# Performance work log

Hardware: AMD Instinct MI355X
Metric: run time of the kernel (lower is better)

## Reference

```python
import jax, jax.numpy as jnp
import numpy as np

K_SIZE = 5  # local window size (odd, SAME padding, stride 1)


def _local_attn(x_main, x_ref, W_main, W_ref, k_size=K_SIZE):
    # 1x1 convs == per-pixel channel matmuls
    cm = jnp.einsum('bhwc,cd->bhwd', x_main, W_main)  # query  [B,H,W,C']
    cr = jnp.einsum('bhwc,cd->bhwd', x_ref, W_ref)    # keys   [B,H,W,C']
    pad = (k_size - 1) // 2
    B, H, W, C = cr.shape
    crp = jnp.pad(cr, ((0, 0), (pad, pad), (pad, pad), (0, 0)))
    # score for each of the k*k offsets: dot(query, shifted key) per pixel.
    # Avoids materializing the [B,H,W,k*k,C] patch tensor.
    scores = [
        jnp.einsum('bhwc,bhwc->bhw', cm, crp[:, i:i + H, j:j + W, :])
        for i in range(k_size) for j in range(k_size)
    ]
    # the layer concatenates the query itself as the last "key" (self score)
    scores.append(jnp.einsum('bhwc,bhwc->bhw', cm, cm))
    attn = jnp.stack(scores, axis=-1)  # [B,H,W,k*k+1]
    return jax.nn.softmax(attn, axis=-1)


def setup_inputs() -> dict:
    key = jax.random.key(0)
    k1, k2, k3, k4 = jax.random.split(key, 4)
    B, H, W, C = 4, 128, 128, 64
    Ci = 64  # intermediate_dim
    return {
        'x_main': jax.random.normal(k1, (B, H, W, C), jnp.float32),
        'x_ref': jax.random.normal(k2, (B, H, W, C), jnp.float32),
        'W_main': jax.random.normal(k3, (C, Ci), jnp.float32) * (2.0 / C) ** 0.5,
        'W_ref': jax.random.normal(k4, (C, Ci), jnp.float32) * (2.0 / C) ** 0.5,
    }


def reference(x_main, x_ref, W_main, W_ref):
    return _local_attn(x_main, x_ref, W_main, W_ref)
```

## Files before the change

kernel.cpp:

```cpp
#include <hip/hip_runtime.h>
#include <math.h>

#define HDIM 128
#define WDIM 128
#define CDIM 64
#define BDIM 4

#define TILE_W 16
#define TILE_H 8
#define HALO_W 20
#define HALO_H 12
#define NHALO (HALO_W * HALO_H)
#define PSTRIDE 68

typedef short bf16x8 __attribute__((ext_vector_type(8)));
typedef float f32x4  __attribute__((ext_vector_type(4)));

__device__ __forceinline__ void split_bf16(float f, short& hi, short& lo) {
    unsigned u = __float_as_uint(f);
    hi = (short)(u >> 16);
    float hf = __uint_as_float(u & 0xffff0000u);
    float l  = f - hf;
    lo = (short)(__float_as_uint(l) >> 16);
}

__device__ __forceinline__ void build_A(const float4 p0, const float4 p1,
                                        const float4 p2, const float4 p3,
                                        bf16x8 Ahi[2], bf16x8 Alo[2]) {
    float fv[16] = {p0.x,p0.y,p0.z,p0.w, p1.x,p1.y,p1.z,p1.w,
                    p2.x,p2.y,p2.z,p2.w, p3.x,p3.y,p3.z,p3.w};
    #pragma unroll
    for (int ks = 0; ks < 2; ++ks)
        #pragma unroll
        for (int j = 0; j < 8; ++j) {
            short hi, lo; split_bf16(fv[8 * ks + j], hi, lo);
            Ahi[ks][j] = hi; Alo[ks][j] = lo;
        }
}

__global__ __launch_bounds__(256, 2)
void fused_mfma_local_attn(const float* __restrict__ xm,
                           const float* __restrict__ xr,
                           const float* __restrict__ Wm,
                           const float* __restrict__ Wr,
                           float* __restrict__ out) {
    __shared__ float lds[16320];
    float* cms = lds;
    float* crs = lds;

    const int t    = threadIdx.x;
    const int lane = t & 63;
    const int wv   = t >> 6;
    const int m    = lane & 15;
    const int quad = lane >> 4;
    const int tx0  = blockIdx.x * TILE_W;
    const int ty0  = blockIdx.y * TILE_H;
    const int b    = blockIdx.z;

    float4 am[2][4];
    #pragma unroll
    for (int s = 0; s < 2; ++s) {
        const int tile = 2 * wv + s;
        const float* ap = xm + (((size_t)b * HDIM + ty0 + tile) * WDIM
                                + tx0 + m) * CDIM + quad * 8;
        am[s][0] = *(const float4*)(ap);
        am[s][1] = *(const float4*)(ap + 4);
        am[s][2] = *(const float4*)(ap + 32);
        am[s][3] = *(const float4*)(ap + 36);
    }

    float4 ar[2][4];
    #pragma unroll
    for (int s = 0; s < 2; ++s) {
        const int tj = wv + 4 * s;
        const int hp = tj * 16 + m;
        const int hy = hp / HALO_W;
        const int hx = hp - hy * HALO_W;
        const int gy = ty0 + hy - 2, gx = tx0 + hx - 2;
        float4 z = make_float4(0.f, 0.f, 0.f, 0.f);
        ar[s][0] = z; ar[s][1] = z; ar[s][2] = z; ar[s][3] = z;
        if (gy >= 0 && gy < HDIM && gx >= 0 && gx < WDIM) {
            const float* ap = xr + (((size_t)b * HDIM + gy) * WDIM + gx) * CDIM
                              + quad * 8;
            ar[s][0] = *(const float4*)(ap);
            ar[s][1] = *(const float4*)(ap + 4);
            ar[s][2] = *(const float4*)(ap + 32);
            ar[s][3] = *(const float4*)(ap + 36);
        }
    }

    bf16x8 Bhi[2][4], Blo[2][4];
    #pragma unroll
    for (int ks = 0; ks < 2; ++ks)
        #pragma unroll
        for (int nt = 0; nt < 4; ++nt)
            #pragma unroll
            for (int j = 0; j < 8; ++j) {
                float f = Wm[(ks * 32 + quad * 8 + j) * CDIM + nt * 16 + m];
                short hi, lo; split_bf16(f, hi, lo);
                Bhi[ks][nt][j] = hi; Blo[ks][nt][j] = lo;
            }

    #pragma unroll
    for (int s = 0; s < 2; ++s) {
        const int tile = 2 * wv + s;
        bf16x8 Ahi[2], Alo[2];
        build_A(am[s][0], am[s][1], am[s][2], am[s][3], Ahi, Alo);
        f32x4 acc[4];
        #pragma unroll
        for (int nt = 0; nt < 4; ++nt)
            { acc[nt][0]=0.f; acc[nt][1]=0.f; acc[nt][2]=0.f; acc[nt][3]=0.f; }
        #pragma unroll
        for (int ks = 0; ks < 2; ++ks)
            #pragma unroll
            for (int nt = 0; nt < 4; ++nt) {
                acc[nt] = __builtin_amdgcn_mfma_f32_16x16x32_bf16(Ahi[ks], Bhi[ks][nt], acc[nt], 0,0,0);
                acc[nt] = __builtin_amdgcn_mfma_f32_16x16x32_bf16(Ahi[ks], Blo[ks][nt], acc[nt], 0,0,0);
                acc[nt] = __builtin_amdgcn_mfma_f32_16x16x32_bf16(Alo[ks], Bhi[ks][nt], acc[nt], 0,0,0);
            }
        #pragma unroll
        for (int nt = 0; nt < 4; ++nt)
            #pragma unroll
            for (int r = 0; r < 4; ++r)
                cms[(tile * 16 + quad * 4 + r) * PSTRIDE + nt * 16 + m] = acc[nt][r];
    }

    const int pl = t >> 1;
    const int cg = t & 1;
    float4 qv[8];
    #pragma unroll
    for (int mq = 0; mq < 8; ++mq)
        qv[mq] = *(const float4*)&cms[pl * PSTRIDE + cg * 32 + 4 * mq];

    float4 ar2[2][4];
    #pragma unroll
    for (int s = 0; s < 2; ++s) {
        const int tj = wv + 4 * (s + 2);
        float4 z = make_float4(0.f, 0.f, 0.f, 0.f);
        ar2[s][0] = z; ar2[s][1] = z; ar2[s][2] = z; ar2[s][3] = z;
        if (tj < 15) {
            const int hp = tj * 16 + m;
            const int hy = hp / HALO_W;
            const int hx = hp - hy * HALO_W;
            const int gy = ty0 + hy - 2, gx = tx0 + hx - 2;
            if (gy >= 0 && gy < HDIM && gx >= 0 && gx < WDIM) {
                const float* ap = xr + (((size_t)b * HDIM + gy) * WDIM + gx) * CDIM
                                  + quad * 8;
                ar2[s][0] = *(const float4*)(ap);
                ar2[s][1] = *(const float4*)(ap + 4);
                ar2[s][2] = *(const float4*)(ap + 32);
                ar2[s][3] = *(const float4*)(ap + 36);
            }
        }
    }

    #pragma unroll
    for (int ks = 0; ks < 2; ++ks)
        #pragma unroll
        for (int nt = 0; nt < 4; ++nt)
            #pragma unroll
            for (int j = 0; j < 8; ++j) {
                float f = Wr[(ks * 32 + quad * 8 + j) * CDIM + nt * 16 + m];
                short hi, lo; split_bf16(f, hi, lo);
                Bhi[ks][nt][j] = hi; Blo[ks][nt][j] = lo;
            }

    __syncthreads();

    #pragma unroll
    for (int s = 0; s < 4; ++s) {
        const int tj = wv + 4 * s;
        if (tj < 15) {
            const float4* pa = (s < 2) ? ar[s] : ar2[s - 2];
            bf16x8 Ahi[2], Alo[2];
            build_A(pa[0], pa[1], pa[2], pa[3], Ahi, Alo);
            f32x4 acc[4];
            #pragma unroll
            for (int nt = 0; nt < 4; ++nt)
                { acc[nt][0]=0.f; acc[nt][1]=0.f; acc[nt][2]=0.f; acc[nt][3]=0.f; }
            #pragma unroll
            for (int ks = 0; ks < 2; ++ks)
                #pragma unroll
                for (int nt = 0; nt < 4; ++nt) {
                    acc[nt] = __builtin_amdgcn_mfma_f32_16x16x32_bf16(Ahi[ks], Bhi[ks][nt], acc[nt], 0,0,0);
                    acc[nt] = __builtin_amdgcn_mfma_f32_16x16x32_bf16(Ahi[ks], Blo[ks][nt], acc[nt], 0,0,0);
                    acc[nt] = __builtin_amdgcn_mfma_f32_16x16x32_bf16(Alo[ks], Bhi[ks][nt], acc[nt], 0,0,0);
                }
            #pragma unroll
            for (int nt = 0; nt < 4; ++nt)
                #pragma unroll
                for (int r = 0; r < 4; ++r)
                    crs[(tj * 16 + quad * 4 + r) * PSTRIDE + nt * 16 + m] = acc[nt][r];
        }
    }
    __syncthreads();

    const int lx = pl & (TILE_W - 1);
    const int ly = pl >> 4;
    const size_t gpx = ((size_t)b * HDIM + ty0 + ly) * WDIM + tx0 + lx;

    float s[26];
    #pragma unroll
    for (int k = 0; k < 25; ++k) {
        const int i = k / 5, j = k % 5;
        const int p = (ly + i) * HALO_W + (lx + j);
        const float4* kp = (const float4*)&crs[p * PSTRIDE + cg * 32];
        float acc = 0.f;
        #pragma unroll
        for (int mq = 0; mq < 8; ++mq) {
            float4 v = kp[mq];
            acc = fmaf(qv[mq].x, v.x, acc);
            acc = fmaf(qv[mq].y, v.y, acc);
            acc = fmaf(qv[mq].z, v.z, acc);
            acc = fmaf(qv[mq].w, v.w, acc);
        }
        s[k] = acc;
    }
    {
        float acc = 0.f;
        #pragma unroll
        for (int mq = 0; mq < 8; ++mq) {
            float4 v = qv[mq];
            acc = fmaf(v.x, v.x, acc);
            acc = fmaf(v.y, v.y, acc);
            acc = fmaf(v.z, v.z, acc);
            acc = fmaf(v.w, v.w, acc);
        }
        s[25] = acc;
    }

    #pragma unroll
    for (int k = 0; k < 26; ++k) s[k] += __shfl_xor(s[k], 1);

    float mx = s[0];
    #pragma unroll
    for (int k = 1; k < 26; ++k) mx = fmaxf(mx, s[k]);
    float sum = 0.f;
    #pragma unroll
    for (int k = 0; k < 26; ++k) { s[k] = __expf(s[k] - mx); sum += s[k]; }
    const float inv = 1.f / sum;

    float* op = &out[gpx * 26 + cg * 13];
    if (cg == 0) {
        #pragma unroll
        for (int k = 0; k < 13; ++k) op[k] = s[k] * inv;
    } else {
        #pragma unroll
        for (int k = 0; k < 13; ++k) op[k] = s[13 + k] * inv;
    }
}

extern "C" void kernel_launch(void* const* d_in, const int* in_sizes, int n_in,
                              void* d_out, int out_size, void* d_ws, size_t ws_size,
                              hipStream_t stream) {
    const float* xm = (const float*)d_in[0];
    const float* xr = (const float*)d_in[1];
    const float* Wm = (const float*)d_in[2];
    const float* Wr = (const float*)d_in[3];
    float* outp = (float*)d_out;

    dim3 g(WDIM / TILE_W, HDIM / TILE_H, BDIM);
    fused_mfma_local_attn<<<g, 256, 0, stream>>>(xm, xr, Wm, Wr, outp);
}
```

Measured before the change: 91.75 us.

## Halve tile height and split channel dot products across four lanes per pixel

The output tile height drops from 8 to 4 rows, so the halo shrinks to 20x8 and the grid has twice as many blocks. Each pixel's 64-channel dot products are now split over four lanes of 16 channels instead of two of 32, reduced with an extra xor shuffle, and each lane writes a quarter of the outputs. Launch bounds ask for 3 blocks per CU. This cuts per-thread register use and LDS size to raise occupancy, at the cost of more redundant halo projection work per output (160 halo pixels for 64 outputs versus 240 for 128) and more shuffles.

```diff
diff --git a/kernel.cpp b/kernel.cpp
--- a/kernel.cpp
+++ b/kernel.cpp
@@ -7,9 +7,9 @@
 #define BDIM 4
 
 #define TILE_W 16
-#define TILE_H 8
+#define TILE_H 4
 #define HALO_W 20
-#define HALO_H 12
+#define HALO_H 8
 #define NHALO (HALO_W * HALO_H)
 #define PSTRIDE 68
 
@@ -38,13 +38,13 @@
         }
 }
 
-__global__ __launch_bounds__(256, 2)
+__global__ __launch_bounds__(256, 3)
 void fused_mfma_local_attn(const float* __restrict__ xm,
                            const float* __restrict__ xr,
                            const float* __restrict__ Wm,
                            const float* __restrict__ Wr,
                            float* __restrict__ out) {
-    __shared__ float lds[16320];
+    __shared__ float lds[NHALO * PSTRIDE];
     float* cms = lds;
     float* crs = lds;
 
@@ -57,16 +57,14 @@
     const int ty0  = blockIdx.y * TILE_H;
     const int b    = blockIdx.z;
 
-    float4 am[2][4];
-    #pragma unroll
-    for (int s = 0; s < 2; ++s) {
-        const int tile = 2 * wv + s;
-        const float* ap = xm + (((size_t)b * HDIM + ty0 + tile) * WDIM
+    float4 am[4];
+    {
+        const float* ap = xm + (((size_t)b * HDIM + ty0 + wv) * WDIM
                                 + tx0 + m) * CDIM + quad * 8;
-        am[s][0] = *(const float4*)(ap);
-        am[s][1] = *(const float4*)(ap + 4);
-        am[s][2] = *(const float4*)(ap + 32);
-        am[s][3] = *(const float4*)(ap + 36);
+        am[0] = *(const float4*)(ap);
+        am[1] = *(const float4*)(ap + 4);
+        am[2] = *(const float4*)(ap + 32);
+        am[3] = *(const float4*)(ap + 36);
     }
 
     float4 ar[2][4];
@@ -101,11 +99,9 @@
                 Bhi[ks][nt][j] = hi; Blo[ks][nt][j] = lo;
             }
 
-    #pragma unroll
-    for (int s = 0; s < 2; ++s) {
-        const int tile = 2 * wv + s;
+    {
         bf16x8 Ahi[2], Alo[2];
-        build_A(am[s][0], am[s][1], am[s][2], am[s][3], Ahi, Alo);
+        build_A(am[0], am[1], am[2], am[3], Ahi, Alo);
         f32x4 acc[4];
         #pragma unroll
         for (int nt = 0; nt < 4; ++nt)
@@ -122,23 +118,22 @@
         for (int nt = 0; nt < 4; ++nt)
             #pragma unroll
             for (int r = 0; r < 4; ++r)
-                cms[(tile * 16 + quad * 4 + r) * PSTRIDE + nt * 16 + m] = acc[nt][r];
-    }
-
-    const int pl = t >> 1;
-    const int cg = t & 1;
-    float4 qv[8];
-    #pragma unroll
-    for (int mq = 0; mq < 8; ++mq)
-        qv[mq] = *(const float4*)&cms[pl * PSTRIDE + cg * 32 + 4 * mq];
-
-    float4 ar2[2][4];
-    #pragma unroll
-    for (int s = 0; s < 2; ++s) {
-        const int tj = wv + 4 * (s + 2);
+                cms[(wv * 16 + quad * 4 + r) * PSTRIDE + nt * 16 + m] = acc[nt][r];
+    }
+
+    const int pl = t >> 2;
+    const int cq = t & 3;
+    float4 qv[4];
+    #pragma unroll
+    for (int mq = 0; mq < 4; ++mq)
+        qv[mq] = *(const float4*)&cms[pl * PSTRIDE + cq * 16 + 4 * mq];
+
+    float4 ar2[4];
+    {
+        const int tj = wv + 8;
         float4 z = make_float4(0.f, 0.f, 0.f, 0.f);
-        ar2[s][0] = z; ar2[s][1] = z; ar2[s][2] = z; ar2[s][3] = z;
-        if (tj < 15) {
+        ar2[0] = z; ar2[1] = z; ar2[2] = z; ar2[3] = z;
+        if (tj < 10) {
             const int hp = tj * 16 + m;
             const int hy = hp / HALO_W;
             const int hx = hp - hy * HALO_W;
@@ -146,10 +141,10 @@
             if (gy >= 0 && gy < HDIM && gx >= 0 && gx < WDIM) {
                 const float* ap = xr + (((size_t)b * HDIM + gy) * WDIM + gx) * CDIM
                                   + quad * 8;
-                ar2[s][0] = *(const float4*)(ap);
-                ar2[s][1] = *(const float4*)(ap + 4);
-                ar2[s][2] = *(const float4*)(ap + 32);
-                ar2[s][3] = *(const float4*)(ap + 36);
+                ar2[0] = *(const float4*)(ap);
+                ar2[1] = *(const float4*)(ap + 4);
+                ar2[2] = *(const float4*)(ap + 32);
+                ar2[3] = *(const float4*)(ap + 36);
             }
         }
     }
@@ -168,10 +163,10 @@
     __syncthreads();
 
     #pragma unroll
-    for (int s = 0; s < 4; ++s) {
+    for (int s = 0; s < 3; ++s) {
         const int tj = wv + 4 * s;
-        if (tj < 15) {
-            const float4* pa = (s < 2) ? ar[s] : ar2[s - 2];
+        if (tj < 10) {
+            const float4* pa = (s < 2) ? ar[s] : ar2;
             bf16x8 Ahi[2], Alo[2];
             build_A(pa[0], pa[1], pa[2], pa[3], Ahi, Alo);
             f32x4 acc[4];
@@ -204,10 +199,10 @@
     for (int k = 0; k < 25; ++k) {
         const int i = k / 5, j = k % 5;
         const int p = (ly + i) * HALO_W + (lx + j);
-        const float4* kp = (const float4*)&crs[p * PSTRIDE + cg * 32];
+        const float4* kp = (const float4*)&crs[p * PSTRIDE + cq * 16];
         float acc = 0.f;
         #pragma unroll
-        for (int mq = 0; mq < 8; ++mq) {
+        for (int mq = 0; mq < 4; ++mq) {
             float4 v = kp[mq];
             acc = fmaf(qv[mq].x, v.x, acc);
             acc = fmaf(qv[mq].y, v.y, acc);
@@ -219,7 +214,7 @@
     {
         float acc = 0.f;
         #pragma unroll
-        for (int mq = 0; mq < 8; ++mq) {
+        for (int mq = 0; mq < 4; ++mq) {
             float4 v = qv[mq];
             acc = fmaf(v.x, v.x, acc);
             acc = fmaf(v.y, v.y, acc);
@@ -231,6 +226,8 @@
 
     #pragma unroll
     for (int k = 0; k < 26; ++k) s[k] += __shfl_xor(s[k], 1);
+    #pragma unroll
+    for (int k = 0; k < 26; ++k) s[k] += __shfl_xor(s[k], 2);
 
     float mx = s[0];
     #pragma unroll
@@ -240,13 +237,19 @@
     for (int k = 0; k < 26; ++k) { s[k] = __expf(s[k] - mx); sum += s[k]; }
     const float inv = 1.f / sum;
 
-    float* op = &out[gpx * 26 + cg * 13];
-    if (cg == 0) {
-        #pragma unroll
-        for (int k = 0; k < 13; ++k) op[k] = s[k] * inv;
+    float* op = &out[gpx * 26];
+    if (cq == 0) {
+        #pragma unroll
+        for (int k = 0; k < 7; ++k) op[k] = s[k] * inv;
+    } else if (cq == 1) {
+        #pragma unroll
+        for (int k = 0; k < 6; ++k) op[7 + k] = s[7 + k] * inv;
+    } else if (cq == 2) {
+        #pragma unroll
+        for (int k = 0; k < 7; ++k) op[13 + k] = s[13 + k] * inv;
     } else {
         #pragma unroll
-        for (int k = 0; k < 13; ++k) op[k] = s[13 + k] * inv;
+        for (int k = 0; k < 6; ++k) op[20 + k] = s[20 + k] * inv;
     }
 }
 
```

Result: slower. 119.9 us (+30.7%).
